# Performance work log

Hardware: AMD Instinct MI355X
Metric: run time of the kernel (lower is better)

The kernel has to match this reference:

```python
import jax, jax.numpy as jnp
import numpy as np

D = 8       # latent dim d
NE = 4      # n_emb
NS = 3      # n_outer stages
NI = 5      # n_inner iterations per stage
EPS = 1e-5  # LayerNorm eps
TAU = 1.0   # route_tau (default), max(1.0, 1e-3) = 1.0


def _ln(x, g, b):
    m = x.mean(-1, keepdims=True)
    v = ((x - m) ** 2).mean(-1, keepdims=True)
    return (x - m) / jnp.sqrt(v + EPS) * g + b


def _inner(E, u, Bm, Wp, bp, W1, b1, W2, b2):
    # E: [B, NE, D], u: [B, D]
    Bsz = E.shape[0]
    # bilinear interaction: outer product e_i u^T + B_i, for all i at once
    M = E[:, :, :, None] * u[:, None, None, :] + Bm[None]      # [B, NE, D, D]
    H = M.reshape(Bsz, NE, D * D) @ Wp.T + bp                  # W_proj: [B, NE, D]
    # softmax routing: s_i = softmax(route(h_i)/tau) over experts
    lg = jax.nn.relu(H @ W1.T + b1) @ W2.T + b2                # [B, NE, NE]
    s = jax.nn.softmax(lg / TAU, axis=-1)
    mix = jnp.einsum('bne,bed->bnd', s, H)                     # per-i mixture of H
    return E + mix


def setup_inputs() -> dict:
    B = 131072
    key = jax.random.key(0)
    ks = jax.random.split(key, 32)
    f32 = jnp.float32
    inp = {
        'cl':     jax.random.normal(ks[0], (B,), f32),
        'cd':     jax.random.normal(ks[1], (B,), f32),
        're_log': jax.random.normal(ks[2], (B,), f32),
        'mach':   jax.random.normal(ks[3], (B,), f32),
        'alpha':  jax.random.normal(ks[4], (B,), f32),
        'u':      jax.random.normal(ks[5], (B, D), f32),
        'We':    jax.random.normal(ks[6], (NE, D, 2), f32) * 0.5,
        'be':    jnp.zeros((NE, D), f32),
        # per-stage InnerBlockAblated params (stacked over NS stages)
        'Bmat':  jax.random.normal(ks[7], (NS, NE, D, D), f32) * 0.05,
        'Wproj': jax.random.normal(ks[8], (NS, D, D * D), f32) * 0.1,
        'bproj': jnp.zeros((NS, D), f32),
        'Wr1':   jax.random.normal(ks[9], (NS, D, D), f32) * 0.3,
        'br1':   jnp.zeros((NS, D), f32),
        'Wr2':   jax.random.normal(ks[10], (NS, NE, D), f32) * 0.3,
        'br2':   jnp.zeros((NS, NE), f32),
        # post-stage LayerNorm
        'ln_g':  jnp.ones((D,), f32),
        'ln_b':  jnp.zeros((D,), f32),
        # final mixing over embeddings: Linear(n_emb*d, n_emb)
        'Wout':  jax.random.normal(ks[11], (NE, NE * D), f32) * 0.1,
        'bout':  jnp.zeros((NE,), f32),
        # final LayerNorm
        'fg':    jnp.ones((D,), f32),
        'fb':    jnp.zeros((D,), f32),
        # heads: head_cst Linear(d, 18), head_cl Linear(d, 1)
        'Wcst':  jax.random.normal(ks[12], (18, D), f32) * 0.2,
        'bcst':  jnp.zeros((18,), f32),
        'Wcl':   jax.random.normal(ks[13], (1, D), f32) * 0.2,
        'bcl':   jnp.zeros((1,), f32),
    }
    return inp


def reference(cl, cd, re_log, mach, alpha, u, We, be, Bmat, Wproj, bproj,
              Wr1, br1, Wr2, br2, ln_g, ln_b, Wout, bout, fg, fb,
              Wcst, bcst, Wcl, bcl):
    # _stack_pairs: [B, 4, 2]
    pairs = jnp.stack([
        jnp.stack([cl, alpha], -1),
        jnp.stack([cd, alpha], -1),
        jnp.stack([re_log, alpha], -1),
        jnp.stack([mach, alpha], -1),
    ], axis=1)
    # embed: per-embedding Linear(2, d) + Tanh  -> E: [B, NE, D]
    E = jnp.tanh(jnp.einsum('bne,nde->bnd', pairs, We) + be[None])
    # outer stages: n_inner inner blocks each, then post-stage LayerNorm
    for s_idx in range(NS):
        for _ in range(NI):
            E = _inner(E, u, Bmat[s_idx], Wproj[s_idx], bproj[s_idx],
                       Wr1[s_idx], br1[s_idx], Wr2[s_idx], br2[s_idx])
        E = _ln(E, ln_g, ln_b)
    # final softmax mixing over embeddings (w_out_logits)
    Bsz = E.shape[0]
    w = jax.nn.softmax(E.reshape(Bsz, NE * D) @ Wout.T + bout, axis=-1)  # [B, NE]
    z = _ln(jnp.einsum('bn,bnd->bd', w, E), fg, fb)                       # [B, D]
    # heads, concatenated: [B, 18 + 1]
    return jnp.concatenate([z @ Wcst.T + bcst, z @ Wcl.T + bcl], axis=-1)
```

## Files before the change

### kernel.cpp

```cpp
#include <hip/hip_runtime.h>

#define D 8
#define NE 4
#define NS 3
#define NI 5
#define LN_EPS 1e-5f

#define OFF_W1  0
#define OFF_W2T 192
#define OFF_B1  288
#define OFF_B2  312
#define OFF_C   324
#define OFF_LN  420
#define OFF_WP  436
#define WLDS_SIZE 1972

typedef float f2 __attribute__((ext_vector_type(2)));

__device__ __forceinline__ f2 fma2(f2 a, f2 b, f2 c) { return __builtin_elementwise_fma(a, b, c); }
__device__ __forceinline__ f2 max2(f2 a, f2 b) { return __builtin_elementwise_max(a, b); }
__device__ __forceinline__ f2 bc(float s) { return (f2){s, s}; }

__global__ void precompute_C_kernel(const float* __restrict__ Bmat,
                                    const float* __restrict__ Wproj,
                                    const float* __restrict__ bproj,
                                    float* __restrict__ C) {
    int idx = threadIdx.x;
    if (idx >= NS * NE * D) return;
    int s = idx / (NE * D);
    int rem = idx % (NE * D);
    int n = rem / D;
    int d = rem % D;
    const float* bm = Bmat + ((size_t)s * NE + n) * 64;
    const float* wp = Wproj + ((size_t)s * D + d) * 64;
    float acc = bproj[s * D + d];
    #pragma unroll
    for (int k = 0; k < 64; ++k) acc += bm[k] * wp[k];
    C[s * 32 + ((n >> 1) * 8 + d) * 2 + (n & 1)] = acc;
}

__device__ __forceinline__ float fast_tanh(float x) {
    float e = __expf(2.f * x);
    return 1.f - 2.f * __builtin_amdgcn_rcpf(e + 1.f);
}

__device__ __forceinline__ float4 ld4(const float* p) {
    return *reinterpret_cast<const float4*>(p);
}

__global__ __launch_bounds__(256, 2) void whisp_kernel(
    const float* __restrict__ cl, const float* __restrict__ cd,
    const float* __restrict__ re_log, const float* __restrict__ mach,
    const float* __restrict__ alpha, const float* __restrict__ u,
    const float* __restrict__ We, const float* __restrict__ be,
    const float* __restrict__ Wproj,
    const float* __restrict__ Wr1, const float* __restrict__ br1,
    const float* __restrict__ Wr2, const float* __restrict__ br2,
    const float* __restrict__ ln_g, const float* __restrict__ ln_b,
    const float* __restrict__ Wout, const float* __restrict__ bout,
    const float* __restrict__ fg, const float* __restrict__ fb,
    const float* __restrict__ Wcst, const float* __restrict__ bcst,
    const float* __restrict__ Wcl, const float* __restrict__ bcl,
    const float* __restrict__ Cpre,
    float* __restrict__ out, int B)
{
    __shared__ __align__(16) float wlds[WLDS_SIZE];
    __shared__ __align__(16) float4 tbuf[16 * 256];

    const int tid = threadIdx.x;
    const int row0 = blockIdx.x * 256 + tid;
    const bool active = (row0 < B);
    const int row = active ? row0 : (B - 1);

    for (int i = tid; i < 192;  i += 256) wlds[OFF_W1 + i] = Wr1[i];
    for (int i = tid; i < 96;   i += 256) {
        int s = i / 32, rem = i % 32, d = rem / 4, e = rem % 4;
        wlds[OFF_W2T + i] = Wr2[s * 32 + e * 8 + d];
    }
    for (int i = tid; i < 24;   i += 256) wlds[OFF_B1 + i] = br1[i];
    for (int i = tid; i < 12;   i += 256) wlds[OFF_B2 + i] = br2[i];
    for (int i = tid; i < 96;   i += 256) wlds[OFF_C + i]  = Cpre[i];
    for (int i = tid; i < 8;    i += 256) { wlds[OFF_LN + i] = ln_g[i]; wlds[OFF_LN + 8 + i] = ln_b[i]; }
    for (int i = tid; i < 1536; i += 256) wlds[OFF_WP + i] = Wproj[i];

    float uu[D];
    {
        const float4* up = reinterpret_cast<const float4*>(u + (size_t)row * D);
        float4 u0 = up[0], u1 = up[1];
        uu[0]=u0.x; uu[1]=u0.y; uu[2]=u0.z; uu[3]=u0.w;
        uu[4]=u1.x; uu[5]=u1.y; uu[6]=u1.z; uu[7]=u1.w;
    }
    float xs[NE] = { cl[row], cd[row], re_log[row], mach[row] };
    float al = alpha[row];

    f2 E2[2][D];
    #pragma unroll
    for (int nn = 0; nn < 2; ++nn) {
        #pragma unroll
        for (int d = 0; d < D; ++d) {
            int na = 2 * nn, nb = 2 * nn + 1;
            float pa = We[na * 16 + d * 2] * xs[na] + We[na * 16 + d * 2 + 1] * al + be[na * D + d];
            float pb = We[nb * 16 + d * 2] * xs[nb] + We[nb * 16 + d * 2 + 1] * al + be[nb * D + d];
            E2[nn][d] = (f2){ fast_tanh(pa), fast_tanh(pb) };
        }
    }

    __syncthreads();

    int zero = 0;

    #pragma unroll 1
    for (int s = 0; s < NS; ++s) {
        {
            const float* Wp = wlds + OFF_WP + s * 512;
            f2 uu2[4] = { {uu[0],uu[1]}, {uu[2],uu[3]}, {uu[4],uu[5]}, {uu[6],uu[7]} };
            #pragma unroll
            for (int d = 0; d < D; ++d) {
                float tv[D];
                #pragma unroll
                for (int i = 0; i < D; ++i) {
                    float4 wa = ld4(Wp + d * 64 + i * 8);
                    float4 wb = ld4(Wp + d * 64 + i * 8 + 4);
                    f2 acc = uu2[0] * (f2){wa.x, wa.y};
                    acc = fma2(uu2[1], (f2){wa.z, wa.w}, acc);
                    acc = fma2(uu2[2], (f2){wb.x, wb.y}, acc);
                    acc = fma2(uu2[3], (f2){wb.z, wb.w}, acc);
                    tv[i] = acc.x + acc.y;
                }
                tbuf[(2 * d) * 256 + tid]     = make_float4(tv[0], tv[1], tv[2], tv[3]);
                tbuf[(2 * d + 1) * 256 + tid] = make_float4(tv[4], tv[5], tv[6], tv[7]);
            }
        }

        float b1a[8], b2a[4];
        {
            float4 q0 = ld4(wlds + OFF_B1 + s * 8);
            float4 q1 = ld4(wlds + OFF_B1 + s * 8 + 4);
            b1a[0]=q0.x; b1a[1]=q0.y; b1a[2]=q0.z; b1a[3]=q0.w;
            b1a[4]=q1.x; b1a[5]=q1.y; b1a[6]=q1.z; b1a[7]=q1.w;
            float4 q2 = ld4(wlds + OFF_B2 + s * 4);
            b2a[0]=q2.x; b2a[1]=q2.y; b2a[2]=q2.z; b2a[3]=q2.w;
        }

        #pragma unroll 1
        for (int it = 0; it < NI; ++it) {
            asm volatile("" : "+v"(zero));
            const float*  W1z  = wlds + OFF_W1  + s * 64 + zero;
            const float*  W2Tz = wlds + OFF_W2T + s * 32 + zero;
            const float*  Cz   = wlds + OFF_C   + s * 32 + zero;
            const float4* tz   = tbuf + tid + zero;

            f2 H2[2][D];
            #pragma unroll
            for (int nn = 0; nn < 2; ++nn) {
                #pragma unroll
                for (int dp = 0; dp < 4; ++dp) {
                    float4 cq = ld4(Cz + nn * 16 + dp * 4);
                    H2[nn][2 * dp]     = (f2){cq.x, cq.y};
                    H2[nn][2 * dp + 1] = (f2){cq.z, cq.w};
                }
            }
            #pragma unroll
            for (int d = 0; d < D; ++d) {
                float4 ta = tz[(2 * d) * 256];
                float4 tb = tz[(2 * d + 1) * 256];
                #pragma unroll
                for (int nn = 0; nn < 2; ++nn) {
                    f2 acc = H2[nn][d];
                    acc = fma2(E2[nn][0], bc(ta.x), acc);
                    acc = fma2(E2[nn][1], bc(ta.y), acc);
                    acc = fma2(E2[nn][2], bc(ta.z), acc);
                    acc = fma2(E2[nn][3], bc(ta.w), acc);
                    acc = fma2(E2[nn][4], bc(tb.x), acc);
                    acc = fma2(E2[nn][5], bc(tb.y), acc);
                    acc = fma2(E2[nn][6], bc(tb.z), acc);
                    acc = fma2(E2[nn][7], bc(tb.w), acc);
                    H2[nn][d] = acc;
                }
            }

            f2 lg2[2][NE];
            #pragma unroll
            for (int nn = 0; nn < 2; ++nn)
                #pragma unroll
                for (int e = 0; e < NE; ++e) lg2[nn][e] = bc(b2a[e]);

            #pragma unroll
            for (int d = 0; d < D; ++d) {
                float4 wa = ld4(W1z + d * 8);
                float4 wb = ld4(W1z + d * 8 + 4);
                float4 w2 = ld4(W2Tz + d * 4);
                #pragma unroll
                for (int nn = 0; nn < 2; ++nn) {
                    f2 acc = bc(b1a[d]);
                    acc = fma2(H2[nn][0], bc(wa.x), acc);
                    acc = fma2(H2[nn][1], bc(wa.y), acc);
                    acc = fma2(H2[nn][2], bc(wa.z), acc);
                    acc = fma2(H2[nn][3], bc(wa.w), acc);
                    acc = fma2(H2[nn][4], bc(wb.x), acc);
                    acc = fma2(H2[nn][5], bc(wb.y), acc);
                    acc = fma2(H2[nn][6], bc(wb.z), acc);
                    acc = fma2(H2[nn][7], bc(wb.w), acc);
                    f2 r2 = max2(acc, bc(0.f));
                    lg2[nn][0] = fma2(r2, bc(w2.x), lg2[nn][0]);
                    lg2[nn][1] = fma2(r2, bc(w2.y), lg2[nn][1]);
                    lg2[nn][2] = fma2(r2, bc(w2.z), lg2[nn][2]);
                    lg2[nn][3] = fma2(r2, bc(w2.w), lg2[nn][3]);
                }
            }

            f2 sm2[2][NE];
            #pragma unroll
            for (int nn = 0; nn < 2; ++nn) {
                f2 m2 = max2(max2(lg2[nn][0], lg2[nn][1]), max2(lg2[nn][2], lg2[nn][3]));
                f2 ee[NE];
                #pragma unroll
                for (int e = 0; e < NE; ++e) {
                    f2 t = lg2[nn][e] - m2;
                    ee[e] = (f2){ __expf(t.x), __expf(t.y) };
                }
                f2 s2 = (ee[0] + ee[1]) + (ee[2] + ee[3]);
                f2 inv2 = (f2){ __builtin_amdgcn_rcpf(s2.x), __builtin_amdgcn_rcpf(s2.y) };
                #pragma unroll
                for (int e = 0; e < NE; ++e) sm2[nn][e] = ee[e] * inv2;
            }

            #pragma unroll
            for (int d = 0; d < D; ++d) {
                #pragma unroll
                for (int nn = 0; nn < 2; ++nn) {
                    f2 acc = E2[nn][d];
                    acc = fma2(sm2[nn][0], bc(H2[0][d].x), acc);
                    acc = fma2(sm2[nn][1], bc(H2[0][d].y), acc);
                    acc = fma2(sm2[nn][2], bc(H2[1][d].x), acc);
                    acc = fma2(sm2[nn][3], bc(H2[1][d].y), acc);
                    E2[nn][d] = acc;
                }
            }
        }

        float lngv[8], lnbv[8];
        {
            float4 g0 = ld4(wlds + OFF_LN),     g1 = ld4(wlds + OFF_LN + 4);
            float4 b0 = ld4(wlds + OFF_LN + 8), b1 = ld4(wlds + OFF_LN + 12);
            lngv[0]=g0.x; lngv[1]=g0.y; lngv[2]=g0.z; lngv[3]=g0.w;
            lngv[4]=g1.x; lngv[5]=g1.y; lngv[6]=g1.z; lngv[7]=g1.w;
            lnbv[0]=b0.x; lnbv[1]=b0.y; lnbv[2]=b0.z; lnbv[3]=b0.w;
            lnbv[4]=b1.x; lnbv[5]=b1.y; lnbv[6]=b1.z; lnbv[7]=b1.w;
        }
        #pragma unroll
        for (int nn = 0; nn < 2; ++nn) {
            f2 s2 = (E2[nn][0] + E2[nn][1]) + (E2[nn][2] + E2[nn][3]);
            s2 = s2 + (E2[nn][4] + E2[nn][5]) + (E2[nn][6] + E2[nn][7]);
            f2 m2 = s2 * bc(0.125f);
            f2 v2 = bc(0.f);
            #pragma unroll
            for (int d = 0; d < D; ++d) { f2 c = E2[nn][d] - m2; v2 = fma2(c, c, v2); }
            v2 = v2 * bc(0.125f);
            f2 inv2 = (f2){ __builtin_amdgcn_rsqf(v2.x + LN_EPS),
                            __builtin_amdgcn_rsqf(v2.y + LN_EPS) };
            #pragma unroll
            for (int d = 0; d < D; ++d)
                E2[nn][d] = fma2((E2[nn][d] - m2) * inv2, bc(lngv[d]), bc(lnbv[d]));
        }
    }

    float lgf[NE];
    #pragma unroll
    for (int e = 0; e < NE; ++e) {
        float a0 = bout[e], a1 = 0.f;
        #pragma unroll
        for (int d = 0; d < D; ++d) {
            a0 = fmaf(E2[0][d].x, Wout[e * 32 + 0 * D + d], a0);
            a1 = fmaf(E2[0][d].y, Wout[e * 32 + 1 * D + d], a1);
            a0 = fmaf(E2[1][d].x, Wout[e * 32 + 2 * D + d], a0);
            a1 = fmaf(E2[1][d].y, Wout[e * 32 + 3 * D + d], a1);
        }
        lgf[e] = a0 + a1;
    }
    float mx = fmaxf(fmaxf(lgf[0], lgf[1]), fmaxf(lgf[2], lgf[3]));
    float w0 = __expf(lgf[0] - mx), w1 = __expf(lgf[1] - mx);
    float w2 = __expf(lgf[2] - mx), w3 = __expf(lgf[3] - mx);
    float winv = __builtin_amdgcn_rcpf((w0 + w1) + (w2 + w3));
    w0 *= winv; w1 *= winv; w2 *= winv; w3 *= winv;

    float z[D];
    #pragma unroll
    for (int d = 0; d < D; ++d) {
        float a0 = w0 * E2[0][d].x;
        float a1 = w1 * E2[0][d].y;
        a0 = fmaf(w2, E2[1][d].x, a0);
        a1 = fmaf(w3, E2[1][d].y, a1);
        z[d] = a0 + a1;
    }
    float zm = 0.f;
    #pragma unroll
    for (int d = 0; d < D; ++d) zm += z[d];
    zm *= (1.f / D);
    float zv = 0.f;
    #pragma unroll
    for (int d = 0; d < D; ++d) { float c = z[d] - zm; zv = fmaf(c, c, zv); }
    zv *= (1.f / D);
    float zinv = __builtin_amdgcn_rsqf(zv + LN_EPS);
    #pragma unroll
    for (int d = 0; d < D; ++d)
        z[d] = (z[d] - zm) * zinv * fg[d] + fb[d];

    float zout[19];
    #pragma unroll
    for (int k = 0; k < 18; ++k) {
        float a0 = bcst[k], a1 = 0.f;
        #pragma unroll
        for (int d = 0; d < D; d += 2) {
            a0 = fmaf(z[d],     Wcst[k * D + d],     a0);
            a1 = fmaf(z[d + 1], Wcst[k * D + d + 1], a1);
        }
        zout[k] = a0 + a1;
    }
    {
        float a0 = bcl[0], a1 = 0.f;
        #pragma unroll
        for (int d = 0; d < D; d += 2) {
            a0 = fmaf(z[d],     Wcl[d],     a0);
            a1 = fmaf(z[d + 1], Wcl[d + 1], a1);
        }
        zout[18] = a0 + a1;
    }

    __syncthreads();
    float* souts = reinterpret_cast<float*>(tbuf);
    if (active) {
        #pragma unroll
        for (int k = 0; k < 19; ++k) souts[tid * 19 + k] = zout[k];
    }
    __syncthreads();

    const int base = blockIdx.x * 256;
    int nrows = B - base;
    if (nrows > 256) nrows = 256;
    if (nrows > 0) {
        const int cnt = nrows * 19;
        for (int i = tid; i < cnt; i += 256)
            out[(size_t)base * 19 + i] = souts[i];
    }
}

extern "C" void kernel_launch(void* const* d_in, const int* in_sizes, int n_in,
                              void* d_out, int out_size, void* d_ws, size_t ws_size,
                              hipStream_t stream) {
    const float* cl     = (const float*)d_in[0];
    const float* cd     = (const float*)d_in[1];
    const float* re_log = (const float*)d_in[2];
    const float* mach   = (const float*)d_in[3];
    const float* alpha  = (const float*)d_in[4];
    const float* u      = (const float*)d_in[5];
    const float* We     = (const float*)d_in[6];
    const float* be     = (const float*)d_in[7];
    const float* Bmat   = (const float*)d_in[8];
    const float* Wproj  = (const float*)d_in[9];
    const float* bproj  = (const float*)d_in[10];
    const float* Wr1    = (const float*)d_in[11];
    const float* br1    = (const float*)d_in[12];
    const float* Wr2    = (const float*)d_in[13];
    const float* br2    = (const float*)d_in[14];
    const float* ln_g   = (const float*)d_in[15];
    const float* ln_b   = (const float*)d_in[16];
    const float* Wout   = (const float*)d_in[17];
    const float* bout   = (const float*)d_in[18];
    const float* fg     = (const float*)d_in[19];
    const float* fb     = (const float*)d_in[20];
    const float* Wcst   = (const float*)d_in[21];
    const float* bcst   = (const float*)d_in[22];
    const float* Wcl    = (const float*)d_in[23];
    const float* bcl    = (const float*)d_in[24];

    float* Cpre = (float*)d_ws;
    const int B = in_sizes[0];

    hipLaunchKernelGGL(precompute_C_kernel, dim3(1), dim3(128), 0, stream,
                       Bmat, Wproj, bproj, Cpre);

    const int blocks = (B + 255) / 256;
    hipLaunchKernelGGL(whisp_kernel, dim3(blocks), dim3(256), 0, stream,
                       cl, cd, re_log, mach, alpha, u, We, be, Wproj,
                       Wr1, br1, Wr2, br2, ln_g, ln_b, Wout, bout, fg, fb,
                       Wcst, bcst, Wcl, bcl, Cpre, (float*)d_out, B);
}
```

Measured before the change: 65.21 us.

## Keep per-stage T matrix in registers instead of LDS, stage u in LDS

The per-stage 8x8 matrix T (u contracted with Wproj) now stays in 64 registers across the inner iterations instead of being written to and re-read from a 64KB per-block LDS buffer. The u vector is parked in LDS so it does not hold registers, the bias loads move inside the inner loop, and the output staging gets its own buffer so one barrier can be dropped. This removes 16 LDS float4 reads per thread per iteration and cuts LDS use, which may let more blocks fit per CU, in exchange for higher register pressure and a possible occupancy loss or spills.

Result: faster. 62.29 us (-4.5%).

```diff
diff --git a/kernel.cpp b/kernel.cpp
--- a/kernel.cpp
+++ b/kernel.cpp
@@ -65,7 +65,8 @@
     float* __restrict__ out, int B)
 {
     __shared__ __align__(16) float wlds[WLDS_SIZE];
-    __shared__ __align__(16) float4 tbuf[16 * 256];
+    __shared__ __align__(16) float4 ubuf[2 * 256];
+    __shared__ float souts[256 * 19];
 
     const int tid = threadIdx.x;
     const int row0 = blockIdx.x * 256 + tid;
@@ -83,12 +84,10 @@
     for (int i = tid; i < 8;    i += 256) { wlds[OFF_LN + i] = ln_g[i]; wlds[OFF_LN + 8 + i] = ln_b[i]; }
     for (int i = tid; i < 1536; i += 256) wlds[OFF_WP + i] = Wproj[i];
 
-    float uu[D];
     {
         const float4* up = reinterpret_cast<const float4*>(u + (size_t)row * D);
-        float4 u0 = up[0], u1 = up[1];
-        uu[0]=u0.x; uu[1]=u0.y; uu[2]=u0.z; uu[3]=u0.w;
-        uu[4]=u1.x; uu[5]=u1.y; uu[6]=u1.z; uu[7]=u1.w;
+        ubuf[tid]       = up[0];
+        ubuf[256 + tid] = up[1];
     }
     float xs[NE] = { cl[row], cd[row], re_log[row], mach[row] };
     float al = alpha[row];
@@ -111,12 +110,13 @@
 
     #pragma unroll 1
     for (int s = 0; s < NS; ++s) {
+        float t[D][D];
         {
+            float4 uq0 = ubuf[tid], uq1 = ubuf[256 + tid];
+            f2 uu2[4] = { {uq0.x,uq0.y}, {uq0.z,uq0.w}, {uq1.x,uq1.y}, {uq1.z,uq1.w} };
             const float* Wp = wlds + OFF_WP + s * 512;
-            f2 uu2[4] = { {uu[0],uu[1]}, {uu[2],uu[3]}, {uu[4],uu[5]}, {uu[6],uu[7]} };
             #pragma unroll
             for (int d = 0; d < D; ++d) {
-                float tv[D];
                 #pragma unroll
                 for (int i = 0; i < D; ++i) {
                     float4 wa = ld4(Wp + d * 64 + i * 8);
@@ -125,30 +125,19 @@
                     acc = fma2(uu2[1], (f2){wa.z, wa.w}, acc);
                     acc = fma2(uu2[2], (f2){wb.x, wb.y}, acc);
                     acc = fma2(uu2[3], (f2){wb.z, wb.w}, acc);
-                    tv[i] = acc.x + acc.y;
-                }
-                tbuf[(2 * d) * 256 + tid]     = make_float4(tv[0], tv[1], tv[2], tv[3]);
-                tbuf[(2 * d + 1) * 256 + tid] = make_float4(tv[4], tv[5], tv[6], tv[7]);
-            }
-        }
-
-        float b1a[8], b2a[4];
-        {
-            float4 q0 = ld4(wlds + OFF_B1 + s * 8);
-            float4 q1 = ld4(wlds + OFF_B1 + s * 8 + 4);
-            b1a[0]=q0.x; b1a[1]=q0.y; b1a[2]=q0.z; b1a[3]=q0.w;
-            b1a[4]=q1.x; b1a[5]=q1.y; b1a[6]=q1.z; b1a[7]=q1.w;
-            float4 q2 = ld4(wlds + OFF_B2 + s * 4);
-            b2a[0]=q2.x; b2a[1]=q2.y; b2a[2]=q2.z; b2a[3]=q2.w;
+                    t[d][i] = acc.x + acc.y;
+                }
+            }
         }
 
         #pragma unroll 1
         for (int it = 0; it < NI; ++it) {
             asm volatile("" : "+v"(zero));
-            const float*  W1z  = wlds + OFF_W1  + s * 64 + zero;
-            const float*  W2Tz = wlds + OFF_W2T + s * 32 + zero;
-            const float*  Cz   = wlds + OFF_C   + s * 32 + zero;
-            const float4* tz   = tbuf + tid + zero;
+            const float* W1z  = wlds + OFF_W1  + s * 64 + zero;
+            const float* W2Tz = wlds + OFF_W2T + s * 32 + zero;
+            const float* Cz   = wlds + OFF_C   + s * 32 + zero;
+            const float* B1z  = wlds + OFF_B1  + s * 8  + zero;
+            const float* B2z  = wlds + OFF_B2  + s * 4  + zero;
 
             f2 H2[2][D];
             #pragma unroll
@@ -162,21 +151,29 @@
             }
             #pragma unroll
             for (int d = 0; d < D; ++d) {
-                float4 ta = tz[(2 * d) * 256];
-                float4 tb = tz[(2 * d + 1) * 256];
                 #pragma unroll
                 for (int nn = 0; nn < 2; ++nn) {
                     f2 acc = H2[nn][d];
-                    acc = fma2(E2[nn][0], bc(ta.x), acc);
-                    acc = fma2(E2[nn][1], bc(ta.y), acc);
-                    acc = fma2(E2[nn][2], bc(ta.z), acc);
-                    acc = fma2(E2[nn][3], bc(ta.w), acc);
-                    acc = fma2(E2[nn][4], bc(tb.x), acc);
-                    acc = fma2(E2[nn][5], bc(tb.y), acc);
-                    acc = fma2(E2[nn][6], bc(tb.z), acc);
-                    acc = fma2(E2[nn][7], bc(tb.w), acc);
+                    acc = fma2(E2[nn][0], bc(t[d][0]), acc);
+                    acc = fma2(E2[nn][1], bc(t[d][1]), acc);
+                    acc = fma2(E2[nn][2], bc(t[d][2]), acc);
+                    acc = fma2(E2[nn][3], bc(t[d][3]), acc);
+                    acc = fma2(E2[nn][4], bc(t[d][4]), acc);
+                    acc = fma2(E2[nn][5], bc(t[d][5]), acc);
+                    acc = fma2(E2[nn][6], bc(t[d][6]), acc);
+                    acc = fma2(E2[nn][7], bc(t[d][7]), acc);
                     H2[nn][d] = acc;
                 }
+            }
+
+            float b1a[8], b2a[4];
+            {
+                float4 q0 = ld4(B1z);
+                float4 q1 = ld4(B1z + 4);
+                b1a[0]=q0.x; b1a[1]=q0.y; b1a[2]=q0.z; b1a[3]=q0.w;
+                b1a[4]=q1.x; b1a[5]=q1.y; b1a[6]=q1.z; b1a[7]=q1.w;
+                float4 q2 = ld4(B2z);
+                b2a[0]=q2.x; b2a[1]=q2.y; b2a[2]=q2.z; b2a[3]=q2.w;
             }
 
             f2 lg2[2][NE];
@@ -216,8 +213,8 @@
                 f2 ee[NE];
                 #pragma unroll
                 for (int e = 0; e < NE; ++e) {
-                    f2 t = lg2[nn][e] - m2;
-                    ee[e] = (f2){ __expf(t.x), __expf(t.y) };
+                    f2 tt = lg2[nn][e] - m2;
+                    ee[e] = (f2){ __expf(tt.x), __expf(tt.y) };
                 }
                 f2 s2 = (ee[0] + ee[1]) + (ee[2] + ee[3]);
                 f2 inv2 = (f2){ __builtin_amdgcn_rcpf(s2.x), __builtin_amdgcn_rcpf(s2.y) };
@@ -327,8 +324,6 @@
         zout[18] = a0 + a1;
     }
 
-    __syncthreads();
-    float* souts = reinterpret_cast<float*>(tbuf);
     if (active) {
         #pragma unroll
         for (int k = 0; k < 19; ++k) souts[tid * 19 + k] = zout[k];
```
